# Kernel tuning notes

Hardware: AMD Instinct MI355X
Metric: run time of the kernel (lower is better)

The kernel has to match this reference:

```python
import jax, jax.numpy as jnp
import numpy as np

IMAGE_DIM = 224


def setup_inputs() -> dict:
    key = jax.random.key(0)
    k1, k2, k3, k4, k5 = jax.random.split(key, 5)
    N, H, W = 64, IMAGE_DIM, IMAGE_DIM
    im1 = jax.random.normal(k1, (N, 3, H, W), dtype=jnp.float32)
    im2 = jax.random.normal(k2, (N, 3, H, W), dtype=jnp.float32)
    C = jax.random.normal(k3, (N, 2, H, W), dtype=jnp.float32)
    M1 = jax.random.uniform(k4, (N, 1, H, W), dtype=jnp.float32)
    M2 = jax.random.uniform(k5, (N, 1, H, W), dtype=jnp.float32)
    return {"im1": im1, "im2": im2, "C": C, "M1": M1, "M2": M2}


def _grid(dtype):
    # q = [repeat(arange(H), W), tile(arange(W), H)], shape [2, H*W]
    x = jnp.repeat(jnp.arange(IMAGE_DIM), IMAGE_DIM)
    y = jnp.tile(jnp.arange(IMAGE_DIM), IMAGE_DIM)
    return jnp.stack([x, y]).astype(dtype)  # [2, HW]


def _bilinear_sample(imflat, qi):
    # imflat: [N, 3, HW], qi: [N, 2, HW] float coords
    HW = imflat.shape[-1]
    px, py = qi[:, 0], qi[:, 1]  # [N, HW]
    fx, cx = jnp.floor(px), jnp.ceil(px)
    fy, cy = jnp.floor(py), jnp.ceil(py)

    def gather_pixel(nx, ny):
        # weight = prod over axes of (1 - |point - neighbor|)
        w = (1.0 - jnp.abs(px - nx)) * (1.0 - jnp.abs(py - ny))  # [N, HW]
        ind = (nx + IMAGE_DIM * ny).astype(jnp.int32)
        ind = jnp.clip(ind, 0, HW - 1)  # guard against out-of-range neighbors
        pix = jnp.take_along_axis(imflat, ind[:, None, :], axis=2)  # [N, 3, HW]
        return w[:, None, :] * pix

    return (gather_pixel(fx, fy) + gather_pixel(cx, fy)
            + gather_pixel(fx, cy) + gather_pixel(cy * 0 + cx, cy))


def reference(im1, im2, C, M1, M2):
    N, ch, H, W = im1.shape
    HW = H * W
    q = _grid(im1.dtype)[None]              # [1, 2, HW]
    Cflat = C.reshape(N, 2, HW)
    a = _bilinear_sample(im1.reshape(N, ch, HW), q + Cflat).reshape(N, ch, H, W) * M1
    b = _bilinear_sample(im2.reshape(N, ch, HW), q - Cflat).reshape(N, ch, H, W) * M2
    return a + b
```

## Files before the change

kernel.cpp:

```cpp
#include <hip/hip_runtime.h>

#define IMG 224
#define HW (IMG * IMG)
#define TILE 32
#define PAD 4
#define REG (TILE + 2 * PAD)
#define RSA 41
#define TABA (REG * RSA)
#define RSB 44
#define TABB (REG * RSB)

__global__ __launch_bounds__(256, 4) void vm_kernel(
    const float* __restrict__ im1, const float* __restrict__ im2,
    const float* __restrict__ C, const float* __restrict__ M1,
    const float* __restrict__ M2, float* __restrict__ out)
{
    __shared__ float2 tabA[2 * TABA];
    __shared__ float  tabB[2 * TABB];

    const int n    = blockIdx.y;
    const int tile = blockIdx.x;
    const int x0   = (tile / 7) * TILE;
    const int y0   = (tile % 7) * TILE;
    const int t    = threadIdx.x;
    const int xlo  = x0 - PAD;
    const int ylo  = y0 - PAD;
    const int gbase = xlo + IMG * ylo;

    const float* i1n = im1 + (size_t)n * 3 * HW;
    const float* i2n = im2 + (size_t)n * 3 * HW;
    const float* Cn  = C  + (size_t)n * 2 * HW;
    const float* M1n = M1 + (size_t)n * HW;
    const float* M2n = M2 + (size_t)n * HW;

#pragma unroll
    for (int img = 0; img < 2; ++img) {
        const float* src = img ? i2n : i1n;
        float2* TA = tabA + img * TABA;
        float*  TB = tabB + img * TABB;
#pragma unroll
        for (int k = 0; k < 2; ++k) {
            int e = t + 256 * k;
            if (e < 400) {
                int r = e / 10, s = e - r * 10;
                int gi = gbase + IMG * r + 4 * s;
                float4 a, b, c;
                if (gi >= 0 && gi <= HW - 4) {
                    a = *(const float4*)(src + gi);
                    b = *(const float4*)(src + HW + gi);
                    c = *(const float4*)(src + 2 * HW + gi);
                } else {
#pragma unroll
                    for (int i = 0; i < 4; ++i) {
                        int g = min(max(gi + i, 0), HW - 1);
                        ((float*)&a)[i] = src[g];
                        ((float*)&b)[i] = src[HW + g];
                        ((float*)&c)[i] = src[2 * HW + g];
                    }
                }
                float2* dA = TA + r * RSA + 4 * s;
                dA[0] = make_float2(a.x, b.x);
                dA[1] = make_float2(a.y, b.y);
                dA[2] = make_float2(a.z, b.z);
                dA[3] = make_float2(a.w, b.w);
                *(float4*)(TB + r * RSB + 4 * s) = c;
            }
        }
    }

    const int tx  = t >> 3;
    const int ty0 = (t & 7) * 4;
    const int p   = (x0 + tx) * IMG + (y0 + ty0);

    const float4 c0v = *(const float4*)(Cn + p);
    const float4 c1v = *(const float4*)(Cn + HW + p);
    const float4 m1v = *(const float4*)(M1n + p);
    const float4 m2v = *(const float4*)(M2n + p);

    __syncthreads();

    const float xf = (float)(x0 + tx);
    float acc0[4], acc1[4], acc2[4];

#pragma unroll
    for (int i = 0; i < 4; ++i) {
        const float yf  = (float)(y0 + ty0 + i);
        const float cc0 = ((const float*)&c0v)[i];
        const float cc1 = ((const float*)&c1v)[i];
        const float m1i = ((const float*)&m1v)[i];
        const float m2i = ((const float*)&m2v)[i];
        float r0c, r1c, r2c;

        {
            float px = xf + cc0, py = yf + cc1;
            float fx = floorf(px), cx = ceilf(px);
            float fy = floorf(py), cy = ceilf(py);
            float wfx = 1.0f - (px - fx), wcx = 1.0f - (cx - px);
            float wfy = 1.0f - (py - fy), wcy = 1.0f - (cy - py);
            float w0 = wfx * wfy, w1 = wcx * wfy;
            float w2 = wfx * wcy, w3 = wcx * wcy;
            int gx0 = (int)fx, gy0 = (int)fy;
            int dx = (int)cx - gx0, dy = (int)cy - gy0;
            int q0 = gx0 - xlo, r0 = gy0 - ylo;
            int in = (q0 >= 0) & (q0 + dx <= REG - 1) &
                     (r0 >= 0) & (r0 + dy <= REG - 1);
            if (__all(in)) {
                int oA = r0 * RSA + q0;
                int oB = r0 * RSB + q0;
                float2 a0 = tabA[oA],            a1 = tabA[oA + dx];
                float2 a2 = tabA[oA + dy * RSA], a3 = tabA[oA + dx + dy * RSA];
                float  b0 = tabB[oB],            b1 = tabB[oB + dx];
                float  b2 = tabB[oB + dy * RSB], b3 = tabB[oB + dx + dy * RSB];
                r0c = m1i * (w0 * a0.x + w1 * a1.x + w2 * a2.x + w3 * a3.x);
                r1c = m1i * (w0 * a0.y + w1 * a1.y + w2 * a2.y + w3 * a3.y);
                r2c = m1i * (w0 * b0   + w1 * b1   + w2 * b2   + w3 * b3);
            } else {
                int i0 = min(max(gx0      + IMG * gy0,        0), HW - 1);
                int i1 = min(max(gx0 + dx + IMG * gy0,        0), HW - 1);
                int i2 = min(max(gx0      + IMG * (gy0 + dy), 0), HW - 1);
                int i3 = min(max(gx0 + dx + IMG * (gy0 + dy), 0), HW - 1);
                r0c = m1i * (w0 * i1n[i0] + w1 * i1n[i1] +
                             w2 * i1n[i2] + w3 * i1n[i3]);
                r1c = m1i * (w0 * i1n[HW + i0] + w1 * i1n[HW + i1] +
                             w2 * i1n[HW + i2] + w3 * i1n[HW + i3]);
                r2c = m1i * (w0 * i1n[2 * HW + i0] + w1 * i1n[2 * HW + i1] +
                             w2 * i1n[2 * HW + i2] + w3 * i1n[2 * HW + i3]);
            }
        }
        {
            float px = xf - cc0, py = yf - cc1;
            float fx = floorf(px), cx = ceilf(px);
            float fy = floorf(py), cy = ceilf(py);
            float wfx = 1.0f - (px - fx), wcx = 1.0f - (cx - px);
            float wfy = 1.0f - (py - fy), wcy = 1.0f - (cy - py);
            float w0 = wfx * wfy, w1 = wcx * wfy;
            float w2 = wfx * wcy, w3 = wcx * wcy;
            int gx0 = (int)fx, gy0 = (int)fy;
            int dx = (int)cx - gx0, dy = (int)cy - gy0;
            int q0 = gx0 - xlo, r0 = gy0 - ylo;
            int in = (q0 >= 0) & (q0 + dx <= REG - 1) &
                     (r0 >= 0) & (r0 + dy <= REG - 1);
            if (__all(in)) {
                const float2* TA = tabA + TABA;
                const float*  TB = tabB + TABB;
                int oA = r0 * RSA + q0;
                int oB = r0 * RSB + q0;
                float2 a0 = TA[oA],            a1 = TA[oA + dx];
                float2 a2 = TA[oA + dy * RSA], a3 = TA[oA + dx + dy * RSA];
                float  b0 = TB[oB],            b1 = TB[oB + dx];
                float  b2 = TB[oB + dy * RSB], b3 = TB[oB + dx + dy * RSB];
                r0c += m2i * (w0 * a0.x + w1 * a1.x + w2 * a2.x + w3 * a3.x);
                r1c += m2i * (w0 * a0.y + w1 * a1.y + w2 * a2.y + w3 * a3.y);
                r2c += m2i * (w0 * b0   + w1 * b1   + w2 * b2   + w3 * b3);
            } else {
                int i0 = min(max(gx0      + IMG * gy0,        0), HW - 1);
                int i1 = min(max(gx0 + dx + IMG * gy0,        0), HW - 1);
                int i2 = min(max(gx0      + IMG * (gy0 + dy), 0), HW - 1);
                int i3 = min(max(gx0 + dx + IMG * (gy0 + dy), 0), HW - 1);
                r0c += m2i * (w0 * i2n[i0] + w1 * i2n[i1] +
                              w2 * i2n[i2] + w3 * i2n[i3]);
                r1c += m2i * (w0 * i2n[HW + i0] + w1 * i2n[HW + i1] +
                              w2 * i2n[HW + i2] + w3 * i2n[HW + i3]);
                r2c += m2i * (w0 * i2n[2 * HW + i0] + w1 * i2n[2 * HW + i1] +
                              w2 * i2n[2 * HW + i2] + w3 * i2n[2 * HW + i3]);
            }
        }
        acc0[i] = r0c; acc1[i] = r1c; acc2[i] = r2c;
    }

    float* on = out + (size_t)n * 3 * HW;
    *(float4*)(on + p)          = make_float4(acc0[0], acc0[1], acc0[2], acc0[3]);
    *(float4*)(on + HW + p)     = make_float4(acc1[0], acc1[1], acc1[2], acc1[3]);
    *(float4*)(on + 2 * HW + p) = make_float4(acc2[0], acc2[1], acc2[2], acc2[3]);
}

extern "C" void kernel_launch(void* const* d_in, const int* in_sizes, int n_in,
                              void* d_out, int out_size, void* d_ws, size_t ws_size,
                              hipStream_t stream) {
    const float* im1 = (const float*)d_in[0];
    const float* im2 = (const float*)d_in[1];
    const float* C   = (const float*)d_in[2];
    const float* M1  = (const float*)d_in[3];
    const float* M2  = (const float*)d_in[4];
    float* out = (float*)d_out;
    dim3 grid(49, 64);
    vm_kernel<<<grid, 256, 0, stream>>>(im1, im2, C, M1, M2, out);
}
```

Before: 171.2 us.

## Make blocks persistent over tile columns with double-buffered LDS prefetch

Each 512-thread block now walks the seven 32x32 tiles along one column of an image instead of handling a single tile. While it computes the current tile from LDS, it prefetches the next tile's halo (both images) and the next tile's flow and mask values into registers, then writes them into a second LDS buffer. Block IDs are remapped so neighbouring tiles land on the same XCD. Loads and stores of the streaming inputs and output use nontemporal hints. The aim is to hide global-load latency behind compute and reuse the overlapping halo rows, at the cost of fewer blocks (448), more LDS per block, and extra syncs.

```diff
diff --git a/kernel.cpp b/kernel.cpp
--- a/kernel.cpp
+++ b/kernel.cpp
@@ -9,86 +9,59 @@
 #define TABA (REG * RSA)
 #define RSB 44
 #define TABB (REG * RSB)
-
-__global__ __launch_bounds__(256, 4) void vm_kernel(
-    const float* __restrict__ im1, const float* __restrict__ im2,
-    const float* __restrict__ C, const float* __restrict__ M1,
-    const float* __restrict__ M2, float* __restrict__ out)
+#define BUFF 10080
+#define TPT 7
+#define NBLK 448
+#define NXCD 8
+
+typedef float vf2 __attribute__((ext_vector_type(2)));
+
+struct U3 { float4 a, b, c; };
+
+__device__ __forceinline__ U3 load3(const float* __restrict__ src, int gi) {
+    U3 u;
+    if (gi >= 0 && gi <= HW - 4) {
+        u.a = *(const float4*)(src + gi);
+        u.b = *(const float4*)(src + HW + gi);
+        u.c = *(const float4*)(src + 2 * HW + gi);
+    } else {
+#pragma unroll
+        for (int i = 0; i < 4; ++i) {
+            int g = min(max(gi + i, 0), HW - 1);
+            ((float*)&u.a)[i] = src[g];
+            ((float*)&u.b)[i] = src[HW + g];
+            ((float*)&u.c)[i] = src[2 * HW + g];
+        }
+    }
+    return u;
+}
+
+__device__ __forceinline__ void writeU(float* __restrict__ base, int img,
+                                       int r, int s, const U3& u) {
+    float2* dA = (float2*)base + img * TABA + r * RSA + 4 * s;
+    dA[0] = make_float2(u.a.x, u.b.x);
+    dA[1] = make_float2(u.a.y, u.b.y);
+    dA[2] = make_float2(u.a.z, u.b.z);
+    dA[3] = make_float2(u.a.w, u.b.w);
+    *(float4*)(base + 6560 + img * TABB + r * RSB + 4 * s) = u.c;
+}
+
+__device__ __forceinline__ void compute_px(
+    const float* __restrict__ Bf, int xlo, int ylo,
+    float xf, int p, int yfb,
+    vf2 c0v, vf2 c1v, vf2 m1v, vf2 m2v,
+    const float* __restrict__ i1n, const float* __restrict__ i2n,
+    float* __restrict__ on)
 {
-    __shared__ float2 tabA[2 * TABA];
-    __shared__ float  tabB[2 * TABB];
-
-    const int n    = blockIdx.y;
-    const int tile = blockIdx.x;
-    const int x0   = (tile / 7) * TILE;
-    const int y0   = (tile % 7) * TILE;
-    const int t    = threadIdx.x;
-    const int xlo  = x0 - PAD;
-    const int ylo  = y0 - PAD;
-    const int gbase = xlo + IMG * ylo;
-
-    const float* i1n = im1 + (size_t)n * 3 * HW;
-    const float* i2n = im2 + (size_t)n * 3 * HW;
-    const float* Cn  = C  + (size_t)n * 2 * HW;
-    const float* M1n = M1 + (size_t)n * HW;
-    const float* M2n = M2 + (size_t)n * HW;
+    const float2* TA = (const float2*)Bf;
+    const float*  TB = Bf + 6560;
+    float acc0[2], acc1[2], acc2[2];
 
 #pragma unroll
-    for (int img = 0; img < 2; ++img) {
-        const float* src = img ? i2n : i1n;
-        float2* TA = tabA + img * TABA;
-        float*  TB = tabB + img * TABB;
-#pragma unroll
-        for (int k = 0; k < 2; ++k) {
-            int e = t + 256 * k;
-            if (e < 400) {
-                int r = e / 10, s = e - r * 10;
-                int gi = gbase + IMG * r + 4 * s;
-                float4 a, b, c;
-                if (gi >= 0 && gi <= HW - 4) {
-                    a = *(const float4*)(src + gi);
-                    b = *(const float4*)(src + HW + gi);
-                    c = *(const float4*)(src + 2 * HW + gi);
-                } else {
-#pragma unroll
-                    for (int i = 0; i < 4; ++i) {
-                        int g = min(max(gi + i, 0), HW - 1);
-                        ((float*)&a)[i] = src[g];
-                        ((float*)&b)[i] = src[HW + g];
-                        ((float*)&c)[i] = src[2 * HW + g];
-                    }
-                }
-                float2* dA = TA + r * RSA + 4 * s;
-                dA[0] = make_float2(a.x, b.x);
-                dA[1] = make_float2(a.y, b.y);
-                dA[2] = make_float2(a.z, b.z);
-                dA[3] = make_float2(a.w, b.w);
-                *(float4*)(TB + r * RSB + 4 * s) = c;
-            }
-        }
-    }
-
-    const int tx  = t >> 3;
-    const int ty0 = (t & 7) * 4;
-    const int p   = (x0 + tx) * IMG + (y0 + ty0);
-
-    const float4 c0v = *(const float4*)(Cn + p);
-    const float4 c1v = *(const float4*)(Cn + HW + p);
-    const float4 m1v = *(const float4*)(M1n + p);
-    const float4 m2v = *(const float4*)(M2n + p);
-
-    __syncthreads();
-
-    const float xf = (float)(x0 + tx);
-    float acc0[4], acc1[4], acc2[4];
-
-#pragma unroll
-    for (int i = 0; i < 4; ++i) {
-        const float yf  = (float)(y0 + ty0 + i);
-        const float cc0 = ((const float*)&c0v)[i];
-        const float cc1 = ((const float*)&c1v)[i];
-        const float m1i = ((const float*)&m1v)[i];
-        const float m2i = ((const float*)&m2v)[i];
+    for (int i = 0; i < 2; ++i) {
+        const float yf  = (float)(yfb + i);
+        const float cc0 = c0v[i], cc1 = c1v[i];
+        const float m1i = m1v[i], m2i = m2v[i];
         float r0c, r1c, r2c;
 
         {
@@ -105,14 +78,13 @@
             int in = (q0 >= 0) & (q0 + dx <= REG - 1) &
                      (r0 >= 0) & (r0 + dy <= REG - 1);
             if (__all(in)) {
-                int oA = r0 * RSA + q0;
-                int oB = r0 * RSB + q0;
-                float2 a0 = tabA[oA],            a1 = tabA[oA + dx];
-                float2 a2 = tabA[oA + dy * RSA], a3 = tabA[oA + dx + dy * RSA];
-                float  b0 = tabB[oB],            b1 = tabB[oB + dx];
-                float  b2 = tabB[oB + dy * RSB], b3 = tabB[oB + dx + dy * RSB];
-                r0c = m1i * (w0 * a0.x + w1 * a1.x + w2 * a2.x + w3 * a3.x);
-                r1c = m1i * (w0 * a0.y + w1 * a1.y + w2 * a2.y + w3 * a3.y);
+                int oA = r0 * RSA + q0, oB = r0 * RSB + q0;
+                float2 A0 = TA[oA],            A1 = TA[oA + dx];
+                float2 A2 = TA[oA + dy * RSA], A3 = TA[oA + dx + dy * RSA];
+                float  b0 = TB[oB],            b1 = TB[oB + dx];
+                float  b2 = TB[oB + dy * RSB], b3 = TB[oB + dx + dy * RSB];
+                r0c = m1i * (w0 * A0.x + w1 * A1.x + w2 * A2.x + w3 * A3.x);
+                r1c = m1i * (w0 * A0.y + w1 * A1.y + w2 * A2.y + w3 * A3.y);
                 r2c = m1i * (w0 * b0   + w1 * b1   + w2 * b2   + w3 * b3);
             } else {
                 int i0 = min(max(gx0      + IMG * gy0,        0), HW - 1);
@@ -141,16 +113,15 @@
             int in = (q0 >= 0) & (q0 + dx <= REG - 1) &
                      (r0 >= 0) & (r0 + dy <= REG - 1);
             if (__all(in)) {
-                const float2* TA = tabA + TABA;
-                const float*  TB = tabB + TABB;
-                int oA = r0 * RSA + q0;
-                int oB = r0 * RSB + q0;
-                float2 a0 = TA[oA],            a1 = TA[oA + dx];
-                float2 a2 = TA[oA + dy * RSA], a3 = TA[oA + dx + dy * RSA];
-                float  b0 = TB[oB],            b1 = TB[oB + dx];
-                float  b2 = TB[oB + dy * RSB], b3 = TB[oB + dx + dy * RSB];
-                r0c += m2i * (w0 * a0.x + w1 * a1.x + w2 * a2.x + w3 * a3.x);
-                r1c += m2i * (w0 * a0.y + w1 * a1.y + w2 * a2.y + w3 * a3.y);
+                const float2* TA2 = TA + TABA;
+                const float*  TB2 = TB + TABB;
+                int oA = r0 * RSA + q0, oB = r0 * RSB + q0;
+                float2 A0 = TA2[oA],            A1 = TA2[oA + dx];
+                float2 A2 = TA2[oA + dy * RSA], A3 = TA2[oA + dx + dy * RSA];
+                float  b0 = TB2[oB],            b1 = TB2[oB + dx];
+                float  b2 = TB2[oB + dy * RSB], b3 = TB2[oB + dx + dy * RSB];
+                r0c += m2i * (w0 * A0.x + w1 * A1.x + w2 * A2.x + w3 * A3.x);
+                r1c += m2i * (w0 * A0.y + w1 * A1.y + w2 * A2.y + w3 * A3.y);
                 r2c += m2i * (w0 * b0   + w1 * b1   + w2 * b2   + w3 * b3);
             } else {
                 int i0 = min(max(gx0      + IMG * gy0,        0), HW - 1);
@@ -168,10 +139,90 @@
         acc0[i] = r0c; acc1[i] = r1c; acc2[i] = r2c;
     }
 
-    float* on = out + (size_t)n * 3 * HW;
-    *(float4*)(on + p)          = make_float4(acc0[0], acc0[1], acc0[2], acc0[3]);
-    *(float4*)(on + HW + p)     = make_float4(acc1[0], acc1[1], acc1[2], acc1[3]);
-    *(float4*)(on + 2 * HW + p) = make_float4(acc2[0], acc2[1], acc2[2], acc2[3]);
+    vf2 o0 = {acc0[0], acc0[1]};
+    vf2 o1 = {acc1[0], acc1[1]};
+    vf2 o2 = {acc2[0], acc2[1]};
+    __builtin_nontemporal_store(o0, (vf2*)(on + p));
+    __builtin_nontemporal_store(o1, (vf2*)(on + HW + p));
+    __builtin_nontemporal_store(o2, (vf2*)(on + 2 * HW + p));
+}
+
+__global__ __launch_bounds__(512, 4) void vm_kernel(
+    const float* __restrict__ im1, const float* __restrict__ im2,
+    const float* __restrict__ C, const float* __restrict__ M1,
+    const float* __restrict__ M2, float* __restrict__ out)
+{
+    __shared__ __align__(16) float lds[2 * BUFF];
+
+    const int bid  = blockIdx.x;
+    const int b    = (bid & (NXCD - 1)) * (NBLK / NXCD) + (bid >> 3);
+    const int n    = b / 7;
+    const int xcol = b - n * 7;
+
+    const int x0  = xcol * TILE;
+    const int t   = threadIdx.x;
+    const int xlo = x0 - PAD;
+
+    const float* i1n = im1 + (size_t)n * 3 * HW;
+    const float* i2n = im2 + (size_t)n * 3 * HW;
+    const float* Cn  = C  + (size_t)n * 2 * HW;
+    const float* M1n = M1 + (size_t)n * HW;
+    const float* M2n = M2 + (size_t)n * HW;
+    float*       on  = out + (size_t)n * 3 * HW;
+
+    const int tx    = t >> 4;
+    const int ty0   = (t & 15) * 2;
+    const int pbase = (x0 + tx) * IMG + ty0;
+    const float xf  = (float)(x0 + tx);
+
+    const bool a1 = (t < 400);
+    const bool a2 = (t >= 112);
+    const int e1 = t,        r1 = e1 / 10, s1 = e1 - 10 * r1;
+    const int e2 = t - 112,  r2 = e2 / 10, s2 = e2 - 10 * r2;
+
+    {
+        int gb = xlo + IMG * (-PAD);
+        U3 u1, u2;
+        if (a1) u1 = load3(i1n, gb + IMG * r1 + 4 * s1);
+        if (a2) u2 = load3(i2n, gb + IMG * r2 + 4 * s2);
+        if (a1) writeU(lds, 0, r1, s1, u1);
+        if (a2) writeU(lds, 1, r2, s2, u2);
+    }
+    vf2 c0c = __builtin_nontemporal_load((const vf2*)(Cn + pbase));
+    vf2 c1c = __builtin_nontemporal_load((const vf2*)(Cn + HW + pbase));
+    vf2 m1c = __builtin_nontemporal_load((const vf2*)(M1n + pbase));
+    vf2 m2c = __builtin_nontemporal_load((const vf2*)(M2n + pbase));
+    __syncthreads();
+
+#pragma unroll 1
+    for (int k = 0; k < TPT; ++k) {
+        const int ylo = k * TILE - PAD;
+        float* Bc = lds + (k & 1) * BUFF;
+        float* Bn = lds + ((k + 1) & 1) * BUFF;
+
+        U3 v1, v2;
+        vf2 c0n, c1n, m1n, m2n;
+        if (k < TPT - 1) {
+            int gbn = xlo + IMG * (ylo + TILE);
+            if (a1) v1 = load3(i1n, gbn + IMG * r1 + 4 * s1);
+            if (a2) v2 = load3(i2n, gbn + IMG * r2 + 4 * s2);
+            int pn = pbase + (k + 1) * TILE;
+            c0n = __builtin_nontemporal_load((const vf2*)(Cn + pn));
+            c1n = __builtin_nontemporal_load((const vf2*)(Cn + HW + pn));
+            m1n = __builtin_nontemporal_load((const vf2*)(M1n + pn));
+            m2n = __builtin_nontemporal_load((const vf2*)(M2n + pn));
+        }
+
+        compute_px(Bc, xlo, ylo, xf, pbase + k * TILE, k * TILE + ty0,
+                   c0c, c1c, m1c, m2c, i1n, i2n, on);
+
+        if (k < TPT - 1) {
+            if (a1) writeU(Bn, 0, r1, s1, v1);
+            if (a2) writeU(Bn, 1, r2, s2, v2);
+            c0c = c0n; c1c = c1n; m1c = m1n; m2c = m2n;
+        }
+        __syncthreads();
+    }
 }
 
 extern "C" void kernel_launch(void* const* d_in, const int* in_sizes, int n_in,
@@ -183,6 +234,5 @@
     const float* M1  = (const float*)d_in[3];
     const float* M2  = (const float*)d_in[4];
     float* out = (float*)d_out;
-    dim3 grid(49, 64);
-    vm_kernel<<<grid, 256, 0, stream>>>(im1, im2, C, M1, M2, out);
-}
+    vm_kernel<<<dim3(NBLK), 512, 0, stream>>>(im1, im2, C, M1, M2, out);
+}
```

Result: slower. 176.8 us (+3.3%).
